# Kernel optimization log

Measured on AMD Instinct MI355X. Metric: run time of the kernel, lower is better.

The kernel has to match this reference:

```python
import jax, jax.numpy as jnp
import numpy as np

MEMORY_SIZE = 2000
SHAPE = (512, 8, 8)
D = int(np.prod(SHAPE))  # 32768
LAM = 0.0005  # hard-shrink threshold (1/memory_size convention)
EPS = 1e-12   # F.normalize eps


def _l2_normalize(x, axis):
    # matches F.normalize(p=2): x / max(||x||, eps)
    n = jnp.sqrt(jnp.sum(x * x, axis=axis, keepdims=True))
    return x / jnp.maximum(n, EPS)


def _hard_shrink(x):
    return jnp.where(jnp.abs(x) > LAM, x, jnp.zeros_like(x))


def setup_inputs() -> dict:
    key = jax.random.key(0)
    k1, k2 = jax.random.split(key)
    feature = jax.random.normal(k1, (256, *SHAPE), dtype=jnp.float32)
    memory = jax.random.normal(k2, (MEMORY_SIZE, D), dtype=jnp.float32)
    return {"feature": feature, "memory": memory}


def reference(feature, memory):
    B = feature.shape[0]
    flat = feature.reshape(B, -1)                     # [B, D]
    fn = _l2_normalize(flat, axis=1)                  # [B, D]
    mn = _l2_normalize(memory, axis=1)                # [M, D]
    w = jnp.einsum('bd,md->bm', fn, mn)               # cosine similarity [B, M]
    w = jax.nn.softmax(w, axis=1)
    w = _hard_shrink(w)
    w = jax.nn.softmax(w, axis=1)
    mem_feat = jnp.einsum('bm,md->bd', w, memory)     # [B, D]
    mem_feat = mem_feat.reshape(B, *SHAPE)
    return (mem_feat, w)
```

## Files before the change

### kernel.cpp

```cpp
#include <hip/hip_runtime.h>
#include <math.h>


#define D_DIM 32768
#define B_DIM 256
#define M_DIM 2000
#define M_PAD 2048
#define NS1 16
#define KSLAB (D_DIM / NS1)
#define LAM 0.0005f
#define LDB 72

typedef __attribute__((ext_vector_type(8))) short bf16x8;
typedef __attribute__((ext_vector_type(4))) float f32x4;

#define GLOBAL_AS __attribute__((address_space(1)))
#define LDS_AS __attribute__((address_space(3)))

__device__ __forceinline__ void cp_async16(const void* g, void* l) {
  __builtin_amdgcn_global_load_lds((const GLOBAL_AS unsigned int*)g,
                                   (LDS_AS unsigned int*)l, 16, 0, 0);
}

__device__ __forceinline__ unsigned short f2bf(float f) {
  union { float f; unsigned u; } v; v.f = f;
  unsigned r = v.u + 0x7FFFu + ((v.u >> 16) & 1u);
  return (unsigned short)(r >> 16);
}

__global__ __launch_bounds__(256) void zero_kernel(float* __restrict__ p, int n) {
  int i = blockIdx.x * 256 + threadIdx.x;
  if (i < n) p[i] = 0.f;
}

__global__ __launch_bounds__(256) void prep_feat_kernel(const float* __restrict__ src,
                                                        unsigned short* __restrict__ dst,
                                                        float* __restrict__ rn_inv) {
  const size_t row = blockIdx.x;
  const int t = threadIdx.x;
  const float4* p = (const float4*)(src + row * (size_t)D_DIM);
  ushort4* q = (ushort4*)(dst + row * (size_t)D_DIM);
  float s = 0.f;
  for (int i = t; i < D_DIM / 4; i += 256) {
    float4 v = p[i];
    s = fmaf(v.x, v.x, s); s = fmaf(v.y, v.y, s);
    s = fmaf(v.z, v.z, s); s = fmaf(v.w, v.w, s);
    ushort4 b; b.x = f2bf(v.x); b.y = f2bf(v.y); b.z = f2bf(v.z); b.w = f2bf(v.w);
    q[i] = b;
  }
  #pragma unroll
  for (int off = 32; off > 0; off >>= 1) s += __shfl_down(s, off, 64);
  __shared__ float partial[4];
  if ((t & 63) == 0) partial[t >> 6] = s;
  __syncthreads();
  if (t == 0) {
    float tt = partial[0] + partial[1] + partial[2] + partial[3];
    rn_inv[row] = 1.0f / fmaxf(sqrtf(tt), 1e-12f);
  }
}

__global__ __launch_bounds__(256, 2) void gemm1_fused(const unsigned short* __restrict__ F16,
                                                      const float* __restrict__ mem,
                                                      float* __restrict__ Spart,
                                                      float* __restrict__ rnm_sq) {
  __shared__ __align__(16) unsigned short Asm[2][256 * 64];
  __shared__ __align__(16) unsigned short Bsm[64 * LDB];
  const int t = threadIdx.x;
  const int m0 = blockIdx.x * 64;
  const int kbase = blockIdx.y * KSLAB;
  const int wid = t >> 6, lane = t & 63;
  const int lr = lane & 15, kq = lane >> 4;
  const int l8 = lane & 7, lrow = lane >> 3;

  const int brow = t >> 2;
  const int bcol = (t & 3) * 16;
  const int gm = m0 + brow;
  const bool bvalid = gm < M_DIM;
  const float* Bg = mem + (size_t)(bvalid ? gm : 0) * D_DIM + kbase + bcol;

  const unsigned short* Ab = F16 + (size_t)(64 * wid + lrow) * D_DIM + kbase + (l8 ^ lrow) * 8;

  f32x4 acc[4][4] = {};
  float ss = 0.f;

  #pragma unroll
  for (int i = 0; i < 8; i++)
    cp_async16(Ab + (size_t)(8 * i) * D_DIM, &Asm[0][(64 * wid + 8 * i) * 64]);
  float4 v[4];
  #pragma unroll
  for (int j = 0; j < 4; j++) v[j] = *(const float4*)(Bg + 4 * j);

  int cur = 0;
  const int NT = KSLAB / 64;
  for (int kt = 0; kt < NT; kt++) {
    #pragma unroll
    for (int j = 0; j < 4; j++) {
      ss = fmaf(v[j].x, v[j].x, ss); ss = fmaf(v[j].y, v[j].y, ss);
      ss = fmaf(v[j].z, v[j].z, ss); ss = fmaf(v[j].w, v[j].w, ss);
      ushort4 c; c.x = f2bf(v[j].x); c.y = f2bf(v[j].y);
      c.z = f2bf(v[j].z); c.w = f2bf(v[j].w);
      *(ushort4*)&Bsm[brow * LDB + bcol + 4 * j] = c;
    }
    __syncthreads();

    float4 vn[4];
    if (kt + 1 < NT) {
      const int kk = (kt + 1) * 64;
      #pragma unroll
      for (int i = 0; i < 8; i++)
        cp_async16(Ab + kk + (size_t)(8 * i) * D_DIM, &Asm[cur ^ 1][(64 * wid + 8 * i) * 64]);
      #pragma unroll
      for (int j = 0; j < 4; j++) vn[j] = *(const float4*)(Bg + kk + 4 * j);
    }

    bf16x8 bfr[2][4];
    #pragma unroll
    for (int h = 0; h < 2; h++)
      #pragma unroll
      for (int ni = 0; ni < 4; ni++)
        bfr[h][ni] = *(const bf16x8*)&Bsm[(ni * 16 + lr) * LDB + h * 32 + kq * 8];
    #pragma unroll
    for (int mi = 0; mi < 4; mi++) {
      #pragma unroll
      for (int h = 0; h < 2; h++) {
        const int sw = ((h * 4 + kq) ^ (lr & 7)) * 8;
        const bf16x8 af = *(const bf16x8*)&Asm[cur][(wid * 64 + mi * 16 + lr) * 64 + sw];
        #pragma unroll
        for (int ni = 0; ni < 4; ni++)
          acc[mi][ni] = __builtin_amdgcn_mfma_f32_16x16x32_bf16(af, bfr[h][ni], acc[mi][ni], 0, 0, 0);
      }
    }
    __syncthreads();
    if (kt + 1 < NT) {
      #pragma unroll
      for (int j = 0; j < 4; j++) v[j] = vn[j];
    }
    cur ^= 1;
  }

  ss += __shfl_down(ss, 2, 4);
  ss += __shfl_down(ss, 1, 4);
  if ((t & 3) == 0 && bvalid) atomicAdd(&rnm_sq[gm], ss);

  float* Sp = Spart + (size_t)blockIdx.y * (B_DIM * M_PAD);
  #pragma unroll
  for (int mi = 0; mi < 4; mi++) {
    const int b0 = wid * 64 + mi * 16 + kq * 4;
    #pragma unroll
    for (int ni = 0; ni < 4; ni++) {
      const int col = m0 + ni * 16 + lr;
      #pragma unroll
      for (int j = 0; j < 4; j++)
        Sp[(size_t)(b0 + j) * M_PAD + col] = acc[mi][ni][j];
    }
  }
}

__device__ __forceinline__ float block_reduce(float x, bool is_max, float* red,
                                              int wid, int lane) {
  #pragma unroll
  for (int off = 32; off > 0; off >>= 1) {
    float o = __shfl_down(x, off, 64);
    x = is_max ? fmaxf(x, o) : (x + o);
  }
  __syncthreads();
  if (lane == 0) red[wid] = x;
  __syncthreads();
  return is_max ? fmaxf(fmaxf(red[0], red[1]), fmaxf(red[2], red[3]))
                : (red[0] + red[1] + red[2] + red[3]);
}

__global__ __launch_bounds__(256) void softmax_kernel(const float* __restrict__ Spart,
                                                      const float* __restrict__ rnf,
                                                      const float* __restrict__ rnm_sq,
                                                      float* __restrict__ wout,
                                                      unsigned short* __restrict__ wbf) {
  const int b = blockIdx.x;
  const int t = threadIdx.x;
  const int wid = t >> 6, lane = t & 63;
  const float sf = rnf[b];
  __shared__ float red[4];

  float v[8];
  #pragma unroll
  for (int g = 0; g < 2; g++) {
    const int mq = g * 1024 + 4 * t;
    f32x4 a = {0.f, 0.f, 0.f, 0.f};
    #pragma unroll
    for (int s = 0; s < NS1; s++)
      a += *(const f32x4*)&Spart[(size_t)s * (B_DIM * M_PAD) + (size_t)b * M_PAD + mq];
    #pragma unroll
    for (int j = 0; j < 4; j++) {
      const int m = mq + j;
      const float msc = 1.0f / fmaxf(sqrtf(rnm_sq[m]), 1e-12f);
      v[g * 4 + j] = (m < M_DIM) ? a[j] * (sf * msc) : -INFINITY;
    }
  }
  float mx = v[0];
  #pragma unroll
  for (int i = 1; i < 8; i++) mx = fmaxf(mx, v[i]);
  mx = block_reduce(mx, true, red, wid, lane);

  float e[8]; float sum = 0.f;
  #pragma unroll
  for (int i = 0; i < 8; i++) { e[i] = expf(v[i] - mx); sum += e[i]; }
  sum = block_reduce(sum, false, red, wid, lane);
  const float inv = 1.f / sum;

  float s2[8];
  #pragma unroll
  for (int i = 0; i < 8; i++) {
    float w1 = e[i] * inv;
    s2[i] = (w1 > LAM) ? w1 : 0.f;
  }
  float mx2 = 0.f;
  #pragma unroll
  for (int i = 0; i < 8; i++) mx2 = fmaxf(mx2, s2[i]);
  mx2 = block_reduce(mx2, true, red, wid, lane);

  float e2[8]; float sum2 = 0.f;
  #pragma unroll
  for (int g = 0; g < 2; g++)
    #pragma unroll
    for (int j = 0; j < 4; j++) {
      const int i = g * 4 + j;
      const int m = g * 1024 + 4 * t + j;
      e2[i] = (m < M_DIM) ? expf(s2[i] - mx2) : 0.f;
      sum2 += e2[i];
    }
  sum2 = block_reduce(sum2, false, red, wid, lane);
  const float inv2 = 1.f / sum2;

  #pragma unroll
  for (int g = 0; g < 2; g++) {
    const int mq = g * 1024 + 4 * t;
    float4 wq; ushort4 bq;
    float* wp = (float*)&wq;
    #pragma unroll
    for (int j = 0; j < 4; j++) {
      const float w2 = e2[g * 4 + j] * inv2;
      wp[j] = w2;
      ((unsigned short*)&bq)[j] = f2bf(w2);
    }
    if (mq + 3 < M_DIM) *(float4*)&wout[(size_t)b * M_DIM + mq] = wq;
    *(ushort4*)&wbf[(size_t)b * M_PAD + mq] = bq;
  }
}

__global__ __launch_bounds__(256, 2) void gemm2_kernel(const unsigned short* __restrict__ W,
                                                       const float* __restrict__ mem,
                                                       float* __restrict__ C) {
  __shared__ __align__(16) unsigned short Wsm[2][256 * 64];
  __shared__ __align__(16) unsigned short Bt[64 * 64];
  const int t = threadIdx.x;
  const int n0 = blockIdx.x * 64;
  const int wid = t >> 6, lane = t & 63;
  const int lr = lane & 15, kq = lane >> 4;
  const int l8 = lane & 7, lrow = lane >> 3;

  const unsigned short* Wb = W + (size_t)(64 * wid + lrow) * M_PAD + (l8 ^ lrow) * 8;

  const int bn = t & 63;
  const int kc = t >> 6;
  const float* Bg2 = mem + n0 + bn;

  f32x4 acc[4][4] = {};

  #pragma unroll
  for (int i = 0; i < 8; i++)
    cp_async16(Wb + (size_t)(8 * i) * M_PAD, &Wsm[0][(64 * wid + 8 * i) * 64]);
  float bv[16];
  #pragma unroll
  for (int j = 0; j < 16; j++) {
    const int k = kc * 16 + j;
    bv[j] = Bg2[(size_t)k * D_DIM];
  }

  int cur = 0;
  const int NT = M_PAD / 64;
  for (int it = 0; it < NT; it++) {
    bf16x8 kb0, kb1;
    #pragma unroll
    for (int j = 0; j < 8; j++) kb0[j] = (short)f2bf(bv[j]);
    #pragma unroll
    for (int j = 0; j < 8; j++) kb1[j] = (short)f2bf(bv[8 + j]);
    *(bf16x8*)&Bt[bn * 64 + (((kc * 2 + 0) ^ (bn & 7)) * 8)] = kb0;
    *(bf16x8*)&Bt[bn * 64 + (((kc * 2 + 1) ^ (bn & 7)) * 8)] = kb1;
    __syncthreads();

    float bvn[16];
    if (it + 1 < NT) {
      const int kn = it * 64 + 64;
      #pragma unroll
      for (int i = 0; i < 8; i++)
        cp_async16(Wb + kn + (size_t)(8 * i) * M_PAD, &Wsm[cur ^ 1][(64 * wid + 8 * i) * 64]);
      #pragma unroll
      for (int j = 0; j < 16; j++) {
        const int k = kn + kc * 16 + j;
        const int r = (k < M_DIM) ? k : 0;
        bvn[j] = Bg2[(size_t)r * D_DIM];
      }
    }

    bf16x8 bfr[2][4];
    #pragma unroll
    for (int h = 0; h < 2; h++)
      #pragma unroll
      for (int ni = 0; ni < 4; ni++)
        bfr[h][ni] = *(const bf16x8*)&Bt[(ni * 16 + lr) * 64 + (((h * 4 + kq) ^ (lr & 7)) * 8)];
    #pragma unroll
    for (int mi = 0; mi < 4; mi++) {
      #pragma unroll
      for (int h = 0; h < 2; h++) {
        const int sw = ((h * 4 + kq) ^ (lr & 7)) * 8;
        const bf16x8 af = *(const bf16x8*)&Wsm[cur][(wid * 64 + mi * 16 + lr) * 64 + sw];
        #pragma unroll
        for (int ni = 0; ni < 4; ni++)
          acc[mi][ni] = __builtin_amdgcn_mfma_f32_16x16x32_bf16(af, bfr[h][ni], acc[mi][ni], 0, 0, 0);
      }
    }
    __syncthreads();
    if (it + 1 < NT) {
      #pragma unroll
      for (int j = 0; j < 16; j++) bv[j] = bvn[j];
    }
    cur ^= 1;
  }
  #pragma unroll
  for (int mi = 0; mi < 4; mi++) {
    const int b0 = wid * 64 + mi * 16 + kq * 4;
    #pragma unroll
    for (int ni = 0; ni < 4; ni++) {
      const int col = n0 + ni * 16 + lr;
      #pragma unroll
      for (int j = 0; j < 4; j++)
        C[(size_t)(b0 + j) * D_DIM + col] = acc[mi][ni][j];
    }
  }
}

extern "C" void kernel_launch(void* const* d_in, const int* in_sizes, int n_in,
                              void* d_out, int out_size, void* d_ws, size_t ws_size,
                              hipStream_t stream) {
  const float* feature = (const float*)d_in[0];
  const float* memory  = (const float*)d_in[1];
  float* out_feat = (float*)d_out;
  float* out_w = out_feat + (size_t)B_DIM * D_DIM;

  char* ws = (char*)d_ws;
  unsigned short* F16 = (unsigned short*)ws;
  float* Spart        = (float*)(ws + 16777216ull);
  unsigned short* Wbf = (unsigned short*)(ws + 50331648ull);
  float* rnm_sq       = (float*)(ws + 51380224ull);
  float* rnf          = (float*)(ws + 51388416ull);

  zero_kernel<<<(M_PAD + 255) / 256, 256, 0, stream>>>(rnm_sq, M_PAD);
  prep_feat_kernel<<<B_DIM, 256, 0, stream>>>(feature, F16, rnf);
  gemm1_fused<<<dim3(M_PAD / 64, NS1), 256, 0, stream>>>(F16, memory, Spart, rnm_sq);
  softmax_kernel<<<B_DIM, 256, 0, stream>>>(Spart, rnf, rnm_sq, out_w, Wbf);
  gemm2_kernel<<<D_DIM / 64, 256, 0, stream>>>(Wbf, memory, out_feat);
}
```

Before: 492.5 us.

## Store split-K partials in bf16 and remap GEMM1 blocks per XCD

GEMM1 now writes its split-K partial similarity sums as bf16 instead of fp32, halving the partial-buffer traffic written by GEMM1 and read by the softmax kernel. The 2D grid becomes a 1D grid of 512 blocks, remapped so that blocks landing on the same XCD share a K slab of the feature matrix, which should improve L2 reuse of the A operand. The cost is precision: each partial is rounded to bf16 before reduction, which could perturb the cosine similarities that feed the softmax and hard-shrink threshold.

Result: no change. 488.6 us (-0.8%).

```diff
diff --git a/kernel.cpp b/kernel.cpp
--- a/kernel.cpp
+++ b/kernel.cpp
@@ -26,6 +26,11 @@
   union { float f; unsigned u; } v; v.f = f;
   unsigned r = v.u + 0x7FFFu + ((v.u >> 16) & 1u);
   return (unsigned short)(r >> 16);
+}
+
+__device__ __forceinline__ float bf2f(unsigned short h) {
+  union { unsigned u; float f; } v; v.u = ((unsigned)h) << 16;
+  return v.f;
 }
 
 __global__ __launch_bounds__(256) void zero_kernel(float* __restrict__ p, int n) {
@@ -61,13 +66,16 @@
 
 __global__ __launch_bounds__(256, 2) void gemm1_fused(const unsigned short* __restrict__ F16,
                                                       const float* __restrict__ mem,
-                                                      float* __restrict__ Spart,
+                                                      unsigned short* __restrict__ Spart,
                                                       float* __restrict__ rnm_sq) {
   __shared__ __align__(16) unsigned short Asm[2][256 * 64];
   __shared__ __align__(16) unsigned short Bsm[64 * LDB];
   const int t = threadIdx.x;
-  const int m0 = blockIdx.x * 64;
-  const int kbase = blockIdx.y * KSLAB;
+  const int bid = blockIdx.x;
+  const int xcd = bid & 7, slot = bid >> 3;
+  const int ysplit = xcd * 2 + (slot >> 5);
+  const int m0 = (slot & 31) * 64;
+  const int kbase = ysplit * KSLAB;
   const int wid = t >> 6, lane = t & 63;
   const int lr = lane & 15, kq = lane >> 4;
   const int l8 = lane & 7, lrow = lane >> 3;
@@ -142,7 +150,7 @@
   ss += __shfl_down(ss, 1, 4);
   if ((t & 3) == 0 && bvalid) atomicAdd(&rnm_sq[gm], ss);
 
-  float* Sp = Spart + (size_t)blockIdx.y * (B_DIM * M_PAD);
+  unsigned short* Sp = Spart + (size_t)ysplit * (B_DIM * M_PAD);
   #pragma unroll
   for (int mi = 0; mi < 4; mi++) {
     const int b0 = wid * 64 + mi * 16 + kq * 4;
@@ -151,7 +159,7 @@
       const int col = m0 + ni * 16 + lr;
       #pragma unroll
       for (int j = 0; j < 4; j++)
-        Sp[(size_t)(b0 + j) * M_PAD + col] = acc[mi][ni][j];
+        Sp[(size_t)(b0 + j) * M_PAD + col] = f2bf(acc[mi][ni][j]);
     }
   }
 }
@@ -170,7 +178,7 @@
                 : (red[0] + red[1] + red[2] + red[3]);
 }
 
-__global__ __launch_bounds__(256) void softmax_kernel(const float* __restrict__ Spart,
+__global__ __launch_bounds__(256) void softmax_kernel(const unsigned short* __restrict__ Spart,
                                                       const float* __restrict__ rnf,
                                                       const float* __restrict__ rnm_sq,
                                                       float* __restrict__ wout,
@@ -185,15 +193,18 @@
   #pragma unroll
   for (int g = 0; g < 2; g++) {
     const int mq = g * 1024 + 4 * t;
-    f32x4 a = {0.f, 0.f, 0.f, 0.f};
-    #pragma unroll
-    for (int s = 0; s < NS1; s++)
-      a += *(const f32x4*)&Spart[(size_t)s * (B_DIM * M_PAD) + (size_t)b * M_PAD + mq];
+    float a0 = 0.f, a1 = 0.f, a2 = 0.f, a3 = 0.f;
+    #pragma unroll
+    for (int s = 0; s < NS1; s++) {
+      const ushort4 u = *(const ushort4*)&Spart[(size_t)s * (B_DIM * M_PAD) + (size_t)b * M_PAD + mq];
+      a0 += bf2f(u.x); a1 += bf2f(u.y); a2 += bf2f(u.z); a3 += bf2f(u.w);
+    }
+    const float aa[4] = {a0, a1, a2, a3};
     #pragma unroll
     for (int j = 0; j < 4; j++) {
       const int m = mq + j;
       const float msc = 1.0f / fmaxf(sqrtf(rnm_sq[m]), 1e-12f);
-      v[g * 4 + j] = (m < M_DIM) ? a[j] * (sf * msc) : -INFINITY;
+      v[g * 4 + j] = (m < M_DIM) ? aa[j] * (sf * msc) : -INFINITY;
     }
   }
   float mx = v[0];
@@ -349,14 +360,14 @@
 
   char* ws = (char*)d_ws;
   unsigned short* F16 = (unsigned short*)ws;
-  float* Spart        = (float*)(ws + 16777216ull);
+  unsigned short* Spart = (unsigned short*)(ws + 16777216ull);
   unsigned short* Wbf = (unsigned short*)(ws + 50331648ull);
   float* rnm_sq       = (float*)(ws + 51380224ull);
   float* rnf          = (float*)(ws + 51388416ull);
 
   zero_kernel<<<(M_PAD + 255) / 256, 256, 0, stream>>>(rnm_sq, M_PAD);
   prep_feat_kernel<<<B_DIM, 256, 0, stream>>>(feature, F16, rnf);
-  gemm1_fused<<<dim3(M_PAD / 64, NS1), 256, 0, stream>>>(F16, memory, Spart, rnm_sq);
+  gemm1_fused<<<512, 256, 0, stream>>>(F16, memory, Spart, rnm_sq);
   softmax_kernel<<<B_DIM, 256, 0, stream>>>(Spart, rnf, rnm_sq, out_w, Wbf);
   gemm2_kernel<<<D_DIM / 64, 256, 0, stream>>>(Wbf, memory, out_feat);
 }
```
